# Kernel optimization log

Hardware: AMD Instinct MI355X
Metric: run time of the kernel (lower is better)

## Reference

```python
import jax, jax.numpy as jnp
import numpy as np

LN_EPS = 1e-5

def _layernorm(x, g, b):
    mu = jnp.mean(x, axis=-1, keepdims=True)
    var = jnp.var(x, axis=-1, keepdims=True)
    return (x - mu) * jax.lax.rsqrt(var + LN_EPS) * g + b

def setup_inputs() -> dict:
    key = jax.random.key(0)
    ks = jax.random.split(key, 12)
    B, E, R = 32, 64, 36
    Dt, Di, D = 768, 2048, 512
    s = 0.02
    return {
        "text_feats": jax.random.normal(ks[0], (B, E, Dt), jnp.float32),
        "image_feats": jax.random.normal(ks[1], (B, R, Di), jnp.float32),
        "W_text": jax.random.normal(ks[2], (Dt, D), jnp.float32) * s,
        "b_text": jnp.zeros((D,), jnp.float32),
        "g_text": jnp.ones((D,), jnp.float32),
        "beta_text": jnp.zeros((D,), jnp.float32),
        "W_img": jax.random.normal(ks[3], (Di, D), jnp.float32) * s,
        "b_img": jnp.zeros((D,), jnp.float32),
        "g_img": jnp.ones((D,), jnp.float32),
        "beta_img": jnp.zeros((D,), jnp.float32),
        "W1": jax.random.normal(ks[4], (2 * D, D), jnp.float32) * s,
        "b1": jnp.zeros((D,), jnp.float32),
        "W2": jax.random.normal(ks[5], (D, 1), jnp.float32) * s,
        "b2": jnp.zeros((1,), jnp.float32),
    }

def reference(text_feats, image_feats, W_text, b_text, g_text, beta_text,
              W_img, b_img, g_img, beta_img, W1, b1, W2, b2):
    B, E, _ = text_feats.shape
    R = image_feats.shape[1]
    D = W_text.shape[1]
    # projections: Linear -> ReLU -> LayerNorm
    text_aligned = _layernorm(jax.nn.relu(text_feats @ W_text + b_text), g_text, beta_text)   # [B,E,D]
    image_aligned = _layernorm(jax.nn.relu(image_feats @ W_img + b_img), g_img, beta_img)     # [B,R,D]
    # pairwise scorer: split W1 to avoid materializing the [B,E,R,2D] concat
    W1_t, W1_i = W1[:D], W1[D:]
    h_t = text_aligned @ W1_t                 # [B,E,D]
    h_i = image_aligned @ W1_i + b1           # [B,R,D]
    h = jax.nn.relu(h_t[:, :, None, :] + h_i[:, None, :, :])  # [B,E,R,D]
    scores_raw = jnp.squeeze(h @ W2, -1) + b2[0]               # [B,E,R]
    alignment_scores = jax.nn.sigmoid(scores_raw)
    # softmax over flattened (E*R) per batch
    w = jax.nn.softmax(alignment_scores.reshape(B, E * R), axis=1).reshape(B, E, R)
    # weighted sum over regions, mean over entities
    aggregated = jnp.einsum('ber,brd->bd', w, image_aligned) / E   # [B,D]
    return alignment_scores, aggregated
```

## Files before the change

kernel.cpp:

```cpp
#include <hip/hip_runtime.h>
#include <math.h>

#define LN_EPS 1e-5f

typedef __attribute__((ext_vector_type(8))) short bf16x8;
typedef __attribute__((ext_vector_type(4))) float f32x4;
typedef unsigned short ushort_t;
typedef unsigned int uint_t;

__device__ __forceinline__ ushort_t f2bf(float f) {
    uint_t u = __float_as_uint(f);
    u += 0x7FFF + ((u >> 16) & 1);
    return (ushort_t)(u >> 16);
}

__device__ __forceinline__ bf16x8 cvt8(float4 a, float4 b) {
    bf16x8 r;
    r[0] = (short)f2bf(a.x); r[1] = (short)f2bf(a.y);
    r[2] = (short)f2bf(a.z); r[3] = (short)f2bf(a.w);
    r[4] = (short)f2bf(b.x); r[5] = (short)f2bf(b.y);
    r[6] = (short)f2bf(b.z); r[7] = (short)f2bf(b.w);
    return r;
}

__global__ __launch_bounds__(256) void prep_kernel(
    const float* __restrict__ W_text, const float* __restrict__ W_img,
    const float* __restrict__ W1,
    ushort_t* __restrict__ Wt_t, ushort_t* __restrict__ Wi_t,
    ushort_t* __restrict__ W1t_t, ushort_t* __restrict__ W1i_t,
    float* __restrict__ stats)
{
    __shared__ float t[32][33];
    int local = blockIdx.x;
    if (local >= 1920) {
        for (int i = threadIdx.x; i < 6400; i += 256) stats[i] = 0.f;
        return;
    }
    const float* src; ushort_t* dst; int K;
    if      (local < 384)  { src = W_text;         dst = Wt_t;  K = 768;  }
    else if (local < 1408) { src = W_img;          dst = Wi_t;  K = 2048; local -= 384; }
    else if (local < 1664) { src = W1;             dst = W1t_t; K = 512;  local -= 1408; }
    else                   { src = W1 + 512 * 512; dst = W1i_t; K = 512;  local -= 1664; }
    const int ntk = K / 32;
    const int k0 = (local % ntk) * 32;
    const int n0 = (local / ntk) * 32;
    const int x = threadIdx.x % 32, y = threadIdx.x / 32;
    #pragma unroll
    for (int j = 0; j < 4; ++j)
        t[y + 8 * j][x] = src[(size_t)(k0 + y + 8 * j) * 512 + n0 + x];
    __syncthreads();
    #pragma unroll
    for (int j = 0; j < 4; ++j)
        dst[(size_t)(n0 + y + 8 * j) * K + k0 + x] = f2bf(t[x][y + 8 * j]);
}

__global__ __launch_bounds__(256) void proj_kernel(
    const float* __restrict__ A0, const ushort_t* __restrict__ B0,
    const float* __restrict__ bias0, float* __restrict__ C0, int K0,
    const float* __restrict__ A1, const ushort_t* __restrict__ B1,
    const float* __restrict__ bias1, float* __restrict__ C1, int K1,
    float* __restrict__ stats, int ysplit)
{
    __shared__ float red[4][64][64];

    const float* A; const ushort_t* Bt; const float* bias; float* C; int K, srow;
    int yy = blockIdx.y;
    if (yy < ysplit) { A = A0; Bt = B0; bias = bias0; C = C0; K = K0; srow = yy * 64; }
    else { A = A1; Bt = B1; bias = bias1; C = C1; K = K1; yy -= ysplit; srow = 2048 + yy * 64; }

    const int tid  = threadIdx.x;
    const int wave = tid >> 6;
    const int lane = tid & 63;
    const int q    = lane >> 4;
    const int mj   = lane & 15;
    const int brow = yy * 64;
    const int bcol = blockIdx.x * 64;

    const float*    Ab = A  + (size_t)(brow + mj) * K + q * 8;
    const ushort_t* Bb = Bt + (size_t)(bcol + mj) * K + q * 8;
    const int kw0    = wave * (K >> 2);
    const int ksteps = K >> 7;

    f32x4 acc[4][4] = {};

    #pragma unroll 2
    for (int s = 0; s < ksteps; ++s) {
        const int k = kw0 + s * 32;
        bf16x8 af[4], bf[4];
        #pragma unroll
        for (int i = 0; i < 4; ++i) {
            const float* pA = Ab + (size_t)i * 16 * K + k;
            float4 x0 = *(const float4*)pA;
            float4 x1 = *(const float4*)(pA + 4);
            af[i] = cvt8(x0, x1);
            bf[i] = *(const bf16x8*)(Bb + (size_t)i * 16 * K + k);
        }
        #pragma unroll
        for (int mi = 0; mi < 4; ++mi)
            #pragma unroll
            for (int ni = 0; ni < 4; ++ni)
                acc[mi][ni] = __builtin_amdgcn_mfma_f32_16x16x32_bf16(
                    af[mi], bf[ni], acc[mi][ni], 0, 0, 0);
    }

    #pragma unroll
    for (int mi = 0; mi < 4; ++mi)
        #pragma unroll
        for (int ni = 0; ni < 4; ++ni)
            #pragma unroll
            for (int r = 0; r < 4; ++r)
                red[wave][mi * 16 + q * 4 + r][ni * 16 + mj] = acc[mi][ni][r];
    __syncthreads();

    #pragma unroll
    for (int g = 0; g < 4; ++g) {
        const int idx = g * 1024 + tid * 4;
        const int row = idx >> 6, col = idx & 63;
        float4 v0 = *(float4*)&red[0][row][col];
        float4 v1 = *(float4*)&red[1][row][col];
        float4 v2 = *(float4*)&red[2][row][col];
        float4 v3 = *(float4*)&red[3][row][col];
        float4 bv = *(const float4*)&bias[bcol + col];
        float4 o;
        o.x = fmaxf((v0.x + v1.x) + (v2.x + v3.x) + bv.x, 0.f);
        o.y = fmaxf((v0.y + v1.y) + (v2.y + v3.y) + bv.y, 0.f);
        o.z = fmaxf((v0.z + v1.z) + (v2.z + v3.z) + bv.z, 0.f);
        o.w = fmaxf((v0.w + v1.w) + (v2.w + v3.w) + bv.w, 0.f);
        *(float4*)&C[(size_t)(brow + row) * 512 + bcol + col] = o;
        float s  = (o.x + o.y) + (o.z + o.w);
        float ss = (o.x * o.x + o.y * o.y) + (o.z * o.z + o.w * o.w);
        #pragma unroll
        for (int m = 1; m < 16; m <<= 1) {
            s  += __shfl_xor(s, m);
            ss += __shfl_xor(ss, m);
        }
        if ((tid & 15) == 0) {
            atomicAdd(&stats[(size_t)(srow + row) * 2], s);
            atomicAdd(&stats[(size_t)(srow + row) * 2 + 1], ss);
        }
    }
}

__global__ __launch_bounds__(256) void h_kernel(
    const float* __restrict__ A0, const ushort_t* __restrict__ B0,
    const float* __restrict__ bias0, float* __restrict__ C0,
    const float* __restrict__ g0, const float* __restrict__ be0, int soff0,
    const float* __restrict__ A1, const ushort_t* __restrict__ B1,
    const float* __restrict__ bias1, float* __restrict__ C1,
    const float* __restrict__ g1, const float* __restrict__ be1, int soff1,
    const float* __restrict__ stats, int ysplit)
{
    __shared__ float red[4][64][64];

    const float* A; const ushort_t* Bt; const float* bias; float* C;
    const float* g; const float* be; int soff;
    int yy = blockIdx.y;
    if (yy < ysplit) { A = A0; Bt = B0; bias = bias0; C = C0; g = g0; be = be0; soff = soff0; }
    else { A = A1; Bt = B1; bias = bias1; C = C1; g = g1; be = be1; soff = soff1; yy -= ysplit; }

    const int tid  = threadIdx.x;
    const int wave = tid >> 6;
    const int lane = tid & 63;
    const int q    = lane >> 4;
    const int mj   = lane & 15;
    const int brow = yy * 64;
    const int bcol = blockIdx.x * 64;

    float mu[4], rstd[4];
    #pragma unroll
    for (int i = 0; i < 4; ++i) {
        const int row = soff + brow + i * 16 + mj;
        float2 st = *(const float2*)&stats[(size_t)row * 2];
        float m   = st.x * (1.f / 512.f);
        float var = st.y * (1.f / 512.f) - m * m;
        mu[i] = m; rstd[i] = rsqrtf(var + LN_EPS);
    }

    const float*    Ab = A  + (size_t)(brow + mj) * 512 + q * 8;
    const ushort_t* Bb = Bt + (size_t)(bcol + mj) * 512 + q * 8;
    const int kw0 = wave * 128;

    f32x4 acc[4][4] = {};

    #pragma unroll 2
    for (int s = 0; s < 4; ++s) {
        const int k = kw0 + s * 32;
        float4 gv0 = *(const float4*)&g[k + q * 8];
        float4 gv1 = *(const float4*)&g[k + q * 8 + 4];
        float4 bv0 = *(const float4*)&be[k + q * 8];
        float4 bv1 = *(const float4*)&be[k + q * 8 + 4];
        bf16x8 af[4], bf[4];
        #pragma unroll
        for (int i = 0; i < 4; ++i) {
            const float* pA = Ab + (size_t)i * 16 * 512 + k;
            float4 x0 = *(const float4*)pA;
            float4 x1 = *(const float4*)(pA + 4);
            float4 t0, t1;
            t0.x = fmaf((x0.x - mu[i]) * rstd[i], gv0.x, bv0.x);
            t0.y = fmaf((x0.y - mu[i]) * rstd[i], gv0.y, bv0.y);
            t0.z = fmaf((x0.z - mu[i]) * rstd[i], gv0.z, bv0.z);
            t0.w = fmaf((x0.w - mu[i]) * rstd[i], gv0.w, bv0.w);
            t1.x = fmaf((x1.x - mu[i]) * rstd[i], gv1.x, bv1.x);
            t1.y = fmaf((x1.y - mu[i]) * rstd[i], gv1.y, bv1.y);
            t1.z = fmaf((x1.z - mu[i]) * rstd[i], gv1.z, bv1.z);
            t1.w = fmaf((x1.w - mu[i]) * rstd[i], gv1.w, bv1.w);
            af[i] = cvt8(t0, t1);
            bf[i] = *(const bf16x8*)(Bb + (size_t)i * 16 * 512 + k);
        }
        #pragma unroll
        for (int mi = 0; mi < 4; ++mi)
            #pragma unroll
            for (int ni = 0; ni < 4; ++ni)
                acc[mi][ni] = __builtin_amdgcn_mfma_f32_16x16x32_bf16(
                    af[mi], bf[ni], acc[mi][ni], 0, 0, 0);
    }

    #pragma unroll
    for (int mi = 0; mi < 4; ++mi)
        #pragma unroll
        for (int ni = 0; ni < 4; ++ni)
            #pragma unroll
            for (int r = 0; r < 4; ++r)
                red[wave][mi * 16 + q * 4 + r][ni * 16 + mj] = acc[mi][ni][r];
    __syncthreads();

    #pragma unroll
    for (int gq = 0; gq < 4; ++gq) {
        const int idx = gq * 1024 + tid * 4;
        const int row = idx >> 6, col = idx & 63;
        float4 v0 = *(float4*)&red[0][row][col];
        float4 v1 = *(float4*)&red[1][row][col];
        float4 v2 = *(float4*)&red[2][row][col];
        float4 v3 = *(float4*)&red[3][row][col];
        float4 o;
        o.x = (v0.x + v1.x) + (v2.x + v3.x);
        o.y = (v0.y + v1.y) + (v2.y + v3.y);
        o.z = (v0.z + v1.z) + (v2.z + v3.z);
        o.w = (v0.w + v1.w) + (v2.w + v3.w);
        if (bias) {
            float4 bv = *(const float4*)&bias[bcol + col];
            o.x += bv.x; o.y += bv.y; o.z += bv.z; o.w += bv.w;
        }
        *(float4*)&C[(size_t)(brow + row) * 512 + bcol + col] = o;
    }
}

__global__ __launch_bounds__(256) void scores_kernel(
    const float* __restrict__ ht, const float* __restrict__ hi,
    const float* __restrict__ W2, const float* __restrict__ b2,
    float* __restrict__ scores)
{
    const int blk  = blockIdx.x;
    const int b    = blk >> 4;
    const int e0   = (blk & 15) * 4;
    const int tid  = threadIdx.x;
    const int lane = tid & 63;
    const int wave = tid >> 6;

    float htv[4][8], w2v[8];
    #pragma unroll
    for (int e = 0; e < 4; ++e) {
        const float* htp = ht + (size_t)(b * 64 + e0 + e) * 512;
        #pragma unroll
        for (int j = 0; j < 8; ++j) htv[e][j] = htp[lane + 64 * j];
    }
    #pragma unroll
    for (int j = 0; j < 8; ++j) w2v[j] = W2[lane + 64 * j];
    const float bb = b2[0];
    const float* hib = hi + (size_t)b * 36 * 512;

    for (int r = wave; r < 36; r += 4) {
        const float* hir = hib + (size_t)r * 512;
        float hv[8];
        #pragma unroll
        for (int j = 0; j < 8; ++j) hv[j] = hir[lane + 64 * j];
        float a0 = 0.f, a1 = 0.f, a2 = 0.f, a3 = 0.f;
        #pragma unroll
        for (int j = 0; j < 8; ++j) {
            a0 = fmaf(fmaxf(htv[0][j] + hv[j], 0.f), w2v[j], a0);
            a1 = fmaf(fmaxf(htv[1][j] + hv[j], 0.f), w2v[j], a1);
            a2 = fmaf(fmaxf(htv[2][j] + hv[j], 0.f), w2v[j], a2);
            a3 = fmaf(fmaxf(htv[3][j] + hv[j], 0.f), w2v[j], a3);
        }
        #pragma unroll
        for (int off = 32; off; off >>= 1) {
            a0 += __shfl_down(a0, off);
            a1 += __shfl_down(a1, off);
            a2 += __shfl_down(a2, off);
            a3 += __shfl_down(a3, off);
        }
        if (lane == 0) {
            float* sp = scores + (size_t)(b * 64 + e0) * 36 + r;
            sp[0]      = 1.f / (1.f + expf(-(a0 + bb)));
            sp[36]     = 1.f / (1.f + expf(-(a1 + bb)));
            sp[72]     = 1.f / (1.f + expf(-(a2 + bb)));
            sp[108]    = 1.f / (1.f + expf(-(a3 + bb)));
        }
    }
}

__global__ __launch_bounds__(256) void agg_kernel(
    const float* __restrict__ scores, const float* __restrict__ ia_raw,
    const float* __restrict__ stats2,
    const float* __restrict__ g, const float* __restrict__ beta,
    float* __restrict__ outAgg)
{
    const int b   = blockIdx.x;
    const int tid = threadIdx.x;
    const float* sc = scores + (size_t)b * 2304;

    __shared__ float part[4][36];
    __shared__ float wsr[36];
    __shared__ float tmp[36];
    __shared__ float inv_s, c1_s;

    const int e4 = tid >> 6;
    const int r  = tid & 63;
    if (r < 36) {
        float p = 0.f;
        #pragma unroll
        for (int e = 0; e < 16; ++e) p += expf(sc[(e * 4 + e4) * 36 + r]);
        part[e4][r] = p;
    }
    __syncthreads();
    if (tid < 36) wsr[tid] = part[0][tid] + part[1][tid] + part[2][tid] + part[3][tid];
    __syncthreads();
    if (tid < 64) {
        float v = (tid < 36) ? wsr[tid] : 0.f;
        #pragma unroll
        for (int off = 32; off; off >>= 1) v += __shfl_down(v, off);
        if (tid == 0) inv_s = 1.f / (v * 64.f);
    }
    __syncthreads();
    if (tid < 36) {
        const int row = b * 36 + tid;
        float2 st = *(const float2*)&stats2[(size_t)row * 2];
        float m   = st.x * (1.f / 512.f);
        float var = st.y * (1.f / 512.f) - m * m;
        float rs  = rsqrtf(var + LN_EPS);
        float W   = wsr[tid] * inv_s;
        wsr[tid]  = W * rs;
        tmp[tid]  = W * rs * m;
    }
    __syncthreads();
    if (tid < 64) {
        float v = (tid < 36) ? tmp[tid] : 0.f;
        #pragma unroll
        for (int off = 32; off; off >>= 1) v += __shfl_down(v, off);
        if (tid == 0) c1_s = v;
    }
    __syncthreads();
    const float c1 = c1_s;

    const float* ib = ia_raw + (size_t)b * 36 * 512;
    for (int d = tid; d < 512; d += 256) {
        float acc = 0.f;
        #pragma unroll
        for (int rr = 0; rr < 36; ++rr)
            acc = fmaf(wsr[rr], ib[rr * 512 + d], acc);
        outAgg[(size_t)b * 512 + d] = g[d] * (acc - c1) + beta[d] * (1.f / 64.f);
    }
}

extern "C" void kernel_launch(void* const* d_in, const int* in_sizes, int n_in,
                              void* d_out, int out_size, void* d_ws, size_t ws_size,
                              hipStream_t stream)
{
    const float* text      = (const float*)d_in[0];
    const float* image     = (const float*)d_in[1];
    const float* W_text    = (const float*)d_in[2];
    const float* b_text    = (const float*)d_in[3];
    const float* g_text    = (const float*)d_in[4];
    const float* beta_text = (const float*)d_in[5];
    const float* W_img     = (const float*)d_in[6];
    const float* b_img     = (const float*)d_in[7];
    const float* g_img     = (const float*)d_in[8];
    const float* beta_img  = (const float*)d_in[9];
    const float* W1        = (const float*)d_in[10];
    const float* b1        = (const float*)d_in[11];
    const float* W2        = (const float*)d_in[12];
    const float* b2        = (const float*)d_in[13];

    float* out_scores = (float*)d_out;
    float* out_agg    = (float*)d_out + 73728;

    char* ws = (char*)d_ws;
    float*    ta    = (float*)(ws);
    float*    ia    = (float*)(ws + 4194304);
    float*    ht    = (float*)(ws + 6553600);
    float*    hi    = (float*)(ws + 10747904);
    ushort_t* Wt_t  = (ushort_t*)(ws + 13107200);
    ushort_t* Wi_t  = (ushort_t*)(ws + 13893632);
    ushort_t* W1t_t = (ushort_t*)(ws + 15990784);
    ushort_t* W1i_t = (ushort_t*)(ws + 16515072);
    float*    stats = (float*)(ws + 17039360);

    prep_kernel<<<1921, 256, 0, stream>>>(W_text, W_img, W1,
                                          Wt_t, Wi_t, W1t_t, W1i_t, stats);
    proj_kernel<<<dim3(8, 50), 256, 0, stream>>>(
        text, Wt_t, b_text, ta, 768,
        image, Wi_t, b_img, ia, 2048,
        stats, 32);
    h_kernel<<<dim3(8, 50), 256, 0, stream>>>(
        ta, W1t_t, nullptr, ht, g_text, beta_text, 0,
        ia, W1i_t, b1, hi, g_img, beta_img, 2048,
        stats, 32);
    scores_kernel<<<512, 256, 0, stream>>>(ht, hi, W2, b2, out_scores);
    agg_kernel<<<32, 256, 0, stream>>>(out_scores, ia, stats + 4096,
                                       g_img, beta_img, out_agg);
}
```

Baseline: 154.3 us.

## Fuse all stages into one cooperative persistent kernel with grid syncs

```diff
diff --git a/kernel.cpp b/kernel.cpp
--- a/kernel.cpp
+++ b/kernel.cpp
@@ -1,5 +1,8 @@
 #include <hip/hip_runtime.h>
+#include <hip/hip_cooperative_groups.h>
 #include <math.h>
+
+namespace cg = cooperative_groups;
 
 #define LN_EPS 1e-5f
 
@@ -23,342 +26,341 @@
     return r;
 }
 
-__global__ __launch_bounds__(256) void prep_kernel(
-    const float* __restrict__ W_text, const float* __restrict__ W_img,
-    const float* __restrict__ W1,
-    ushort_t* __restrict__ Wt_t, ushort_t* __restrict__ Wi_t,
-    ushort_t* __restrict__ W1t_t, ushort_t* __restrict__ W1i_t,
-    float* __restrict__ stats)
+__global__ void mega_kernel(
+    const float* __restrict__ text, const float* __restrict__ image,
+    const float* __restrict__ W_text, const float* __restrict__ b_text,
+    const float* __restrict__ g_text, const float* __restrict__ beta_text,
+    const float* __restrict__ W_img, const float* __restrict__ b_img,
+    const float* __restrict__ g_img, const float* __restrict__ beta_img,
+    const float* __restrict__ W1, const float* __restrict__ b1,
+    const float* __restrict__ W2, const float* __restrict__ b2,
+    float* __restrict__ out_scores, float* __restrict__ out_agg,
+    char* __restrict__ ws)
 {
-    __shared__ float t[32][33];
-    int local = blockIdx.x;
-    if (local >= 1920) {
-        for (int i = threadIdx.x; i < 6400; i += 256) stats[i] = 0.f;
-        return;
-    }
-    const float* src; ushort_t* dst; int K;
-    if      (local < 384)  { src = W_text;         dst = Wt_t;  K = 768;  }
-    else if (local < 1408) { src = W_img;          dst = Wi_t;  K = 2048; local -= 384; }
-    else if (local < 1664) { src = W1;             dst = W1t_t; K = 512;  local -= 1408; }
-    else                   { src = W1 + 512 * 512; dst = W1i_t; K = 512;  local -= 1664; }
-    const int ntk = K / 32;
-    const int k0 = (local % ntk) * 32;
-    const int n0 = (local / ntk) * 32;
-    const int x = threadIdx.x % 32, y = threadIdx.x / 32;
-    #pragma unroll
-    for (int j = 0; j < 4; ++j)
-        t[y + 8 * j][x] = src[(size_t)(k0 + y + 8 * j) * 512 + n0 + x];
-    __syncthreads();
-    #pragma unroll
-    for (int j = 0; j < 4; ++j)
-        dst[(size_t)(n0 + y + 8 * j) * K + k0 + x] = f2bf(t[x][y + 8 * j]);
-}
-
-__global__ __launch_bounds__(256) void proj_kernel(
-    const float* __restrict__ A0, const ushort_t* __restrict__ B0,
-    const float* __restrict__ bias0, float* __restrict__ C0, int K0,
-    const float* __restrict__ A1, const ushort_t* __restrict__ B1,
-    const float* __restrict__ bias1, float* __restrict__ C1, int K1,
-    float* __restrict__ stats, int ysplit)
-{
-    __shared__ float red[4][64][64];
-
-    const float* A; const ushort_t* Bt; const float* bias; float* C; int K, srow;
-    int yy = blockIdx.y;
-    if (yy < ysplit) { A = A0; Bt = B0; bias = bias0; C = C0; K = K0; srow = yy * 64; }
-    else { A = A1; Bt = B1; bias = bias1; C = C1; K = K1; yy -= ysplit; srow = 2048 + yy * 64; }
-
+    __shared__ __align__(16) float red[4][64][64];
+
+    ushort_t* text_bf  = (ushort_t*)(ws);
+    ushort_t* image_bf = (ushort_t*)(ws + 3145728);
+    float*    ta       = (float*)(ws + 7864320);
+    float*    ia       = (float*)(ws + 12058624);
+    float*    ht       = (float*)(ws + 14417920);
+    float*    hi       = (float*)(ws + 18612224);
+    ushort_t* Wt_t     = (ushort_t*)(ws + 20971520);
+    ushort_t* Wi_t     = (ushort_t*)(ws + 21757952);
+    ushort_t* W1t_t    = (ushort_t*)(ws + 23855104);
+    ushort_t* W1i_t    = (ushort_t*)(ws + 24379392);
+    float*    stats    = (float*)(ws + 24903680);
+
+    cg::grid_group gg = cg::this_grid();
     const int tid  = threadIdx.x;
     const int wave = tid >> 6;
     const int lane = tid & 63;
     const int q    = lane >> 4;
     const int mj   = lane & 15;
-    const int brow = yy * 64;
-    const int bcol = blockIdx.x * 64;
-
-    const float*    Ab = A  + (size_t)(brow + mj) * K + q * 8;
-    const ushort_t* Bb = Bt + (size_t)(bcol + mj) * K + q * 8;
-    const int kw0    = wave * (K >> 2);
-    const int ksteps = K >> 7;
-
-    f32x4 acc[4][4] = {};
-
-    #pragma unroll 2
-    for (int s = 0; s < ksteps; ++s) {
-        const int k = kw0 + s * 32;
-        bf16x8 af[4], bf[4];
+
+    for (int u = blockIdx.x; u < 5761; u += gridDim.x) {
+        if (u < 3840) {
+            const int i4 = u * 1024 + tid * 4;
+            const float* src; ushort_t* dst; int off;
+            if (i4 < 1572864) { src = text;  dst = text_bf;  off = i4; }
+            else              { src = image; dst = image_bf; off = i4 - 1572864; }
+            float4 v = *(const float4*)(src + off);
+            ushort4 o;
+            o.x = f2bf(v.x); o.y = f2bf(v.y); o.z = f2bf(v.z); o.w = f2bf(v.w);
+            *(ushort4*)(dst + off) = o;
+        } else if (u < 5760) {
+            float (*t33)[33] = (float(*)[33])&red[0][0][0];
+            int local = u - 3840;
+            const float* src; ushort_t* dst; int K;
+            if      (local < 384)  { src = W_text;         dst = Wt_t;  K = 768;  }
+            else if (local < 1408) { src = W_img;          dst = Wi_t;  K = 2048; local -= 384; }
+            else if (local < 1664) { src = W1;             dst = W1t_t; K = 512;  local -= 1408; }
+            else                   { src = W1 + 512 * 512; dst = W1i_t; K = 512;  local -= 1664; }
+            const int ntk = K / 32;
+            const int k0 = (local % ntk) * 32;
+            const int n0 = (local / ntk) * 32;
+            const int x = tid % 32, y = tid / 32;
+            __syncthreads();
+            #pragma unroll
+            for (int j = 0; j < 4; ++j)
+                t33[y + 8 * j][x] = src[(size_t)(k0 + y + 8 * j) * 512 + n0 + x];
+            __syncthreads();
+            #pragma unroll
+            for (int j = 0; j < 4; ++j)
+                dst[(size_t)(n0 + y + 8 * j) * K + k0 + x] = f2bf(t33[x][y + 8 * j]);
+        } else {
+            for (int i = tid; i < 6400; i += 256) stats[i] = 0.f;
+        }
+    }
+
+    gg.sync();
+    for (int u = blockIdx.x; u < 400; u += gridDim.x) {
+        const ushort_t* A; const ushort_t* Bt; const float* bias; float* C;
+        int K, srow, yy, xx;
+        if (u < 256) {
+            yy = u >> 3; xx = u & 7;
+            A = text_bf; Bt = Wt_t; bias = b_text; C = ta; K = 768; srow = yy * 64;
+        } else {
+            int v = u - 256; yy = v >> 3; xx = v & 7;
+            A = image_bf; Bt = Wi_t; bias = b_img; C = ia; K = 2048; srow = 2048 + yy * 64;
+        }
+        const int brow = yy * 64, bcol = xx * 64;
+        const ushort_t* Ab = A  + (size_t)(brow + mj) * K + q * 8;
+        const ushort_t* Bb = Bt + (size_t)(bcol + mj) * K + q * 8;
+        const int kw0 = wave * (K >> 2);
+        const int ksteps = K >> 7;
+
+        f32x4 acc[4][4] = {};
+        #pragma unroll 2
+        for (int s = 0; s < ksteps; ++s) {
+            const int k = kw0 + s * 32;
+            bf16x8 af[4], bfr[4];
+            #pragma unroll
+            for (int i = 0; i < 4; ++i) {
+                af[i]  = *(const bf16x8*)(Ab + (size_t)i * 16 * K + k);
+                bfr[i] = *(const bf16x8*)(Bb + (size_t)i * 16 * K + k);
+            }
+            #pragma unroll
+            for (int mi = 0; mi < 4; ++mi)
+                #pragma unroll
+                for (int ni = 0; ni < 4; ++ni)
+                    acc[mi][ni] = __builtin_amdgcn_mfma_f32_16x16x32_bf16(
+                        af[mi], bfr[ni], acc[mi][ni], 0, 0, 0);
+        }
+        #pragma unroll
+        for (int mi = 0; mi < 4; ++mi)
+            #pragma unroll
+            for (int ni = 0; ni < 4; ++ni)
+                #pragma unroll
+                for (int r = 0; r < 4; ++r)
+                    red[wave][mi * 16 + q * 4 + r][ni * 16 + mj] = acc[mi][ni][r];
+        __syncthreads();
+        #pragma unroll
+        for (int g4 = 0; g4 < 4; ++g4) {
+            const int idx = g4 * 1024 + tid * 4;
+            const int row = idx >> 6, col = idx & 63;
+            float4 v0 = *(float4*)&red[0][row][col];
+            float4 v1 = *(float4*)&red[1][row][col];
+            float4 v2 = *(float4*)&red[2][row][col];
+            float4 v3 = *(float4*)&red[3][row][col];
+            float4 bv = *(const float4*)&bias[bcol + col];
+            float4 o;
+            o.x = fmaxf((v0.x + v1.x) + (v2.x + v3.x) + bv.x, 0.f);
+            o.y = fmaxf((v0.y + v1.y) + (v2.y + v3.y) + bv.y, 0.f);
+            o.z = fmaxf((v0.z + v1.z) + (v2.z + v3.z) + bv.z, 0.f);
+            o.w = fmaxf((v0.w + v1.w) + (v2.w + v3.w) + bv.w, 0.f);
+            *(float4*)&C[(size_t)(brow + row) * 512 + bcol + col] = o;
+            float s  = (o.x + o.y) + (o.z + o.w);
+            float ss = (o.x * o.x + o.y * o.y) + (o.z * o.z + o.w * o.w);
+            #pragma unroll
+            for (int m = 1; m < 16; m <<= 1) {
+                s  += __shfl_xor(s, m);
+                ss += __shfl_xor(ss, m);
+            }
+            if ((tid & 15) == 0) {
+                atomicAdd(&stats[(size_t)(srow + row) * 2], s);
+                atomicAdd(&stats[(size_t)(srow + row) * 2 + 1], ss);
+            }
+        }
+        __syncthreads();
+    }
+
+    gg.sync();
+    for (int u = blockIdx.x; u < 400; u += gridDim.x) {
+        const float* A; const ushort_t* Bt; const float* bias; float* C;
+        const float* g; const float* be; int soff, yy, xx;
+        if (u < 256) {
+            yy = u >> 3; xx = u & 7;
+            A = ta; Bt = W1t_t; bias = nullptr; C = ht;
+            g = g_text; be = beta_text; soff = 0;
+        } else {
+            int v = u - 256; yy = v >> 3; xx = v & 7;
+            A = ia; Bt = W1i_t; bias = b1; C = hi;
+            g = g_img; be = beta_img; soff = 2048;
+        }
+        const int brow = yy * 64, bcol = xx * 64;
+
+        float mu[4], rstd[4];
         #pragma unroll
         for (int i = 0; i < 4; ++i) {
-            const float* pA = Ab + (size_t)i * 16 * K + k;
-            float4 x0 = *(const float4*)pA;
-            float4 x1 = *(const float4*)(pA + 4);
-            af[i] = cvt8(x0, x1);
-            bf[i] = *(const bf16x8*)(Bb + (size_t)i * 16 * K + k);
+            const int row = soff + brow + i * 16 + mj;
+            float2 st = *(const float2*)&stats[(size_t)row * 2];
+            float m   = st.x * (1.f / 512.f);
+            float var = st.y * (1.f / 512.f) - m * m;
+            mu[i] = m; rstd[i] = rsqrtf(var + LN_EPS);
+        }
+
+        const float*    Ab = A  + (size_t)(brow + mj) * 512 + q * 8;
+        const ushort_t* Bb = Bt + (size_t)(bcol + mj) * 512 + q * 8;
+        const int kw0 = wave * 128;
+
+        f32x4 acc[4][4] = {};
+        #pragma unroll 2
+        for (int s = 0; s < 4; ++s) {
+            const int k = kw0 + s * 32;
+            float4 gv0 = *(const float4*)&g[k + q * 8];
+            float4 gv1 = *(const float4*)&g[k + q * 8 + 4];
+            float4 bv0 = *(const float4*)&be[k + q * 8];
+            float4 bv1 = *(const float4*)&be[k + q * 8 + 4];
+            bf16x8 af[4], bfr[4];
+            #pragma unroll
+            for (int i = 0; i < 4; ++i) {
+                const float* pA = Ab + (size_t)i * 16 * 512 + k;
+                float4 x0 = *(const float4*)pA;
+                float4 x1 = *(const float4*)(pA + 4);
+                float4 t0, t1;
+                t0.x = fmaf((x0.x - mu[i]) * rstd[i], gv0.x, bv0.x);
+                t0.y = fmaf((x0.y - mu[i]) * rstd[i], gv0.y, bv0.y);
+                t0.z = fmaf((x0.z - mu[i]) * rstd[i], gv0.z, bv0.z);
+                t0.w = fmaf((x0.w - mu[i]) * rstd[i], gv0.w, bv0.w);
+                t1.x = fmaf((x1.x - mu[i]) * rstd[i], gv1.x, bv1.x);
+                t1.y = fmaf((x1.y - mu[i]) * rstd[i], gv1.y, bv1.y);
+                t1.z = fmaf((x1.z - mu[i]) * rstd[i], gv1.z, bv1.z);
+                t1.w = fmaf((x1.w - mu[i]) * rstd[i], gv1.w, bv1.w);
+                af[i]  = cvt8(t0, t1);
+                bfr[i] = *(const bf16x8*)(Bb + (size_t)i * 16 * 512 + k);
+            }
+            #pragma unroll
+            for (int mi = 0; mi < 4; ++mi)
+                #pragma unroll
+                for (int ni = 0; ni < 4; ++ni)
+                    acc[mi][ni] = __builtin_amdgcn_mfma_f32_16x16x32_bf16(
+                        af[mi], bfr[ni], acc[mi][ni], 0, 0, 0);
         }
         #pragma unroll
         for (int mi = 0; mi < 4; ++mi)
             #pragma unroll
             for (int ni = 0; ni < 4; ++ni)
-                acc[mi][ni] = __builtin_amdgcn_mfma_f32_16x16x32_bf16(
-                    af[mi], bf[ni], acc[mi][ni], 0, 0, 0);
-    }
-
-    #pragma unroll
-    for (int mi = 0; mi < 4; ++mi)
-        #pragma unroll
-        for (int ni = 0; ni < 4; ++ni)
-            #pragma unroll
-            for (int r = 0; r < 4; ++r)
-                red[wave][mi * 16 + q * 4 + r][ni * 16 + mj] = acc[mi][ni][r];
-    __syncthreads();
-
-    #pragma unroll
-    for (int g = 0; g < 4; ++g) {
-        const int idx = g * 1024 + tid * 4;
-        const int row = idx >> 6, col = idx & 63;
-        float4 v0 = *(float4*)&red[0][row][col];
-        float4 v1 = *(float4*)&red[1][row][col];
-        float4 v2 = *(float4*)&red[2][row][col];
-        float4 v3 = *(float4*)&red[3][row][col];
-        float4 bv = *(const float4*)&bias[bcol + col];
-        float4 o;
-        o.x = fmaxf((v0.x + v1.x) + (v2.x + v3.x) + bv.x, 0.f);
-        o.y = fmaxf((v0.y + v1.y) + (v2.y + v3.y) + bv.y, 0.f);
-        o.z = fmaxf((v0.z + v1.z) + (v2.z + v3.z) + bv.z, 0.f);
-        o.w = fmaxf((v0.w + v1.w) + (v2.w + v3.w) + bv.w, 0.f);
-        *(float4*)&C[(size_t)(brow + row) * 512 + bcol + col] = o;
-        float s  = (o.x + o.y) + (o.z + o.w);
-        float ss = (o.x * o.x + o.y * o.y) + (o.z * o.z + o.w * o.w);
-        #pragma unroll
-        for (int m = 1; m < 16; m <<= 1) {
-            s  += __shfl_xor(s, m);
-            ss += __shfl_xor(ss, m);
-        }
-        if ((tid & 15) == 0) {
-            atomicAdd(&stats[(size_t)(srow + row) * 2], s);
-            atomicAdd(&stats[(size_t)(srow + row) * 2 + 1], ss);
-        }
-    }
-}
-
-__global__ __launch_bounds__(256) void h_kernel(
-    const float* __restrict__ A0, const ushort_t* __restrict__ B0,
-    const float* __restrict__ bias0, float* __restrict__ C0,
-    const float* __restrict__ g0, const float* __restrict__ be0, int soff0,
-    const float* __restrict__ A1, const ushort_t* __restrict__ B1,
-    const float* __restrict__ bias1, float* __restrict__ C1,
-    const float* __restrict__ g1, const float* __restrict__ be1, int soff1,
-    const float* __restrict__ stats, int ysplit)
-{
-    __shared__ float red[4][64][64];
-
-    const float* A; const ushort_t* Bt; const float* bias; float* C;
-    const float* g; const float* be; int soff;
-    int yy = blockIdx.y;
-    if (yy < ysplit) { A = A0; Bt = B0; bias = bias0; C = C0; g = g0; be = be0; soff = soff0; }
-    else { A = A1; Bt = B1; bias = bias1; C = C1; g = g1; be = be1; soff = soff1; yy -= ysplit; }
-
-    const int tid  = threadIdx.x;
-    const int wave = tid >> 6;
-    const int lane = tid & 63;
-    const int q    = lane >> 4;
-    const int mj   = lane & 15;
-    const int brow = yy * 64;
-    const int bcol = blockIdx.x * 64;
-
-    float mu[4], rstd[4];
-    #pragma unroll
-    for (int i = 0; i < 4; ++i) {
-        const int row = soff + brow + i * 16 + mj;
-        float2 st = *(const float2*)&stats[(size_t)row * 2];
-        float m   = st.x * (1.f / 512.f);
-        float var = st.y * (1.f / 512.f) - m * m;
-        mu[i] = m; rstd[i] = rsqrtf(var + LN_EPS);
-    }
-
-    const float*    Ab = A  + (size_t)(brow + mj) * 512 + q * 8;
-    const ushort_t* Bb = Bt + (size_t)(bcol + mj) * 512 + q * 8;
-    const int kw0 = wave * 128;
-
-    f32x4 acc[4][4] = {};
-
-    #pragma unroll 2
-    for (int s = 0; s < 4; ++s) {
-        const int k = kw0 + s * 32;
-        float4 gv0 = *(const float4*)&g[k + q * 8];
-        float4 gv1 = *(const float4*)&g[k + q * 8 + 4];
-        float4 bv0 = *(const float4*)&be[k + q * 8];
-        float4 bv1 = *(const float4*)&be[k + q * 8 + 4];
-        bf16x8 af[4], bf[4];
-        #pragma unroll
-        for (int i = 0; i < 4; ++i) {
-            const float* pA = Ab + (size_t)i * 16 * 512 + k;
-            float4 x0 = *(const float4*)pA;
-            float4 x1 = *(const float4*)(pA + 4);
-            float4 t0, t1;
-            t0.x = fmaf((x0.x - mu[i]) * rstd[i], gv0.x, bv0.x);
-            t0.y = fmaf((x0.y - mu[i]) * rstd[i], gv0.y, bv0.y);
-            t0.z = fmaf((x0.z - mu[i]) * rstd[i], gv0.z, bv0.z);
-            t0.w = fmaf((x0.w - mu[i]) * rstd[i], gv0.w, bv0.w);
-            t1.x = fmaf((x1.x - mu[i]) * rstd[i], gv1.x, bv1.x);
-            t1.y = fmaf((x1.y - mu[i]) * rstd[i], gv1.y, bv1.y);
-            t1.z = fmaf((x1.z - mu[i]) * rstd[i], gv1.z, bv1.z);
-            t1.w = fmaf((x1.w - mu[i]) * rstd[i], gv1.w, bv1.w);
-            af[i] = cvt8(t0, t1);
-            bf[i] = *(const bf16x8*)(Bb + (size_t)i * 16 * 512 + k);
-        }
-        #pragma unroll
-        for (int mi = 0; mi < 4; ++mi)
-            #pragma unroll
-            for (int ni = 0; ni < 4; ++ni)
-                acc[mi][ni] = __builtin_amdgcn_mfma_f32_16x16x32_bf16(
-                    af[mi], bf[ni], acc[mi][ni], 0, 0, 0);
-    }
-
-    #pragma unroll
-    for (int mi = 0; mi < 4; ++mi)
-        #pragma unroll
-        for (int ni = 0; ni < 4; ++ni)
-            #pragma unroll
-            for (int r = 0; r < 4; ++r)
-                red[wave][mi * 16 + q * 4 + r][ni * 16 + mj] = acc[mi][ni][r];
-    __syncthreads();
-
-    #pragma unroll
-    for (int gq = 0; gq < 4; ++gq) {
-        const int idx = gq * 1024 + tid * 4;
-        const int row = idx >> 6, col = idx & 63;
-        float4 v0 = *(float4*)&red[0][row][col];
-        float4 v1 = *(float4*)&red[1][row][col];
-        float4 v2 = *(float4*)&red[2][row][col];
-        float4 v3 = *(float4*)&red[3][row][col];
-        float4 o;
-        o.x = (v0.x + v1.x) + (v2.x + v3.x);
-        o.y = (v0.y + v1.y) + (v2.y + v3.y);
-        o.z = (v0.z + v1.z) + (v2.z + v3.z);
-        o.w = (v0.w + v1.w) + (v2.w + v3.w);
-        if (bias) {
-            float4 bv = *(const float4*)&bias[bcol + col];
-            o.x += bv.x; o.y += bv.y; o.z += bv.z; o.w += bv.w;
-        }
-        *(float4*)&C[(size_t)(brow + row) * 512 + bcol + col] = o;
-    }
-}
-
-__global__ __launch_bounds__(256) void scores_kernel(
-    const float* __restrict__ ht, const float* __restrict__ hi,
-    const float* __restrict__ W2, const float* __restrict__ b2,
-    float* __restrict__ scores)
-{
-    const int blk  = blockIdx.x;
-    const int b    = blk >> 4;
-    const int e0   = (blk & 15) * 4;
-    const int tid  = threadIdx.x;
-    const int lane = tid & 63;
-    const int wave = tid >> 6;
-
-    float htv[4][8], w2v[8];
-    #pragma unroll
-    for (int e = 0; e < 4; ++e) {
-        const float* htp = ht + (size_t)(b * 64 + e0 + e) * 512;
-        #pragma unroll
-        for (int j = 0; j < 8; ++j) htv[e][j] = htp[lane + 64 * j];
-    }
-    #pragma unroll
-    for (int j = 0; j < 8; ++j) w2v[j] = W2[lane + 64 * j];
-    const float bb = b2[0];
-    const float* hib = hi + (size_t)b * 36 * 512;
-
-    for (int r = wave; r < 36; r += 4) {
-        const float* hir = hib + (size_t)r * 512;
-        float hv[8];
-        #pragma unroll
-        for (int j = 0; j < 8; ++j) hv[j] = hir[lane + 64 * j];
-        float a0 = 0.f, a1 = 0.f, a2 = 0.f, a3 = 0.f;
-        #pragma unroll
-        for (int j = 0; j < 8; ++j) {
-            a0 = fmaf(fmaxf(htv[0][j] + hv[j], 0.f), w2v[j], a0);
-            a1 = fmaf(fmaxf(htv[1][j] + hv[j], 0.f), w2v[j], a1);
-            a2 = fmaf(fmaxf(htv[2][j] + hv[j], 0.f), w2v[j], a2);
-            a3 = fmaf(fmaxf(htv[3][j] + hv[j], 0.f), w2v[j], a3);
-        }
-        #pragma unroll
-        for (int off = 32; off; off >>= 1) {
-            a0 += __shfl_down(a0, off);
-            a1 += __shfl_down(a1, off);
-            a2 += __shfl_down(a2, off);
-            a3 += __shfl_down(a3, off);
-        }
-        if (lane == 0) {
-            float* sp = scores + (size_t)(b * 64 + e0) * 36 + r;
-            sp[0]      = 1.f / (1.f + expf(-(a0 + bb)));
-            sp[36]     = 1.f / (1.f + expf(-(a1 + bb)));
-            sp[72]     = 1.f / (1.f + expf(-(a2 + bb)));
-            sp[108]    = 1.f / (1.f + expf(-(a3 + bb)));
-        }
-    }
-}
-
-__global__ __launch_bounds__(256) void agg_kernel(
-    const float* __restrict__ scores, const float* __restrict__ ia_raw,
-    const float* __restrict__ stats2,
-    const float* __restrict__ g, const float* __restrict__ beta,
-    float* __restrict__ outAgg)
-{
-    const int b   = blockIdx.x;
-    const int tid = threadIdx.x;
-    const float* sc = scores + (size_t)b * 2304;
-
-    __shared__ float part[4][36];
-    __shared__ float wsr[36];
-    __shared__ float tmp[36];
-    __shared__ float inv_s, c1_s;
-
-    const int e4 = tid >> 6;
-    const int r  = tid & 63;
-    if (r < 36) {
-        float p = 0.f;
-        #pragma unroll
-        for (int e = 0; e < 16; ++e) p += expf(sc[(e * 4 + e4) * 36 + r]);
-        part[e4][r] = p;
-    }
-    __syncthreads();
-    if (tid < 36) wsr[tid] = part[0][tid] + part[1][tid] + part[2][tid] + part[3][tid];
-    __syncthreads();
-    if (tid < 64) {
-        float v = (tid < 36) ? wsr[tid] : 0.f;
-        #pragma unroll
-        for (int off = 32; off; off >>= 1) v += __shfl_down(v, off);
-        if (tid == 0) inv_s = 1.f / (v * 64.f);
-    }
-    __syncthreads();
-    if (tid < 36) {
-        const int row = b * 36 + tid;
-        float2 st = *(const float2*)&stats2[(size_t)row * 2];
-        float m   = st.x * (1.f / 512.f);
-        float var = st.y * (1.f / 512.f) - m * m;
-        float rs  = rsqrtf(var + LN_EPS);
-        float W   = wsr[tid] * inv_s;
-        wsr[tid]  = W * rs;
-        tmp[tid]  = W * rs * m;
-    }
-    __syncthreads();
-    if (tid < 64) {
-        float v = (tid < 36) ? tmp[tid] : 0.f;
-        #pragma unroll
-        for (int off = 32; off; off >>= 1) v += __shfl_down(v, off);
-        if (tid == 0) c1_s = v;
-    }
-    __syncthreads();
-    const float c1 = c1_s;
-
-    const float* ib = ia_raw + (size_t)b * 36 * 512;
-    for (int d = tid; d < 512; d += 256) {
-        float acc = 0.f;
-        #pragma unroll
-        for (int rr = 0; rr < 36; ++rr)
-            acc = fmaf(wsr[rr], ib[rr * 512 + d], acc);
-        outAgg[(size_t)b * 512 + d] = g[d] * (acc - c1) + beta[d] * (1.f / 64.f);
+                #pragma unroll
+                for (int r = 0; r < 4; ++r)
+                    red[wave][mi * 16 + q * 4 + r][ni * 16 + mj] = acc[mi][ni][r];
+        __syncthreads();
+        #pragma unroll
+        for (int g4 = 0; g4 < 4; ++g4) {
+            const int idx = g4 * 1024 + tid * 4;
+            const int row = idx >> 6, col = idx & 63;
+            float4 v0 = *(float4*)&red[0][row][col];
+            float4 v1 = *(float4*)&red[1][row][col];
+            float4 v2 = *(float4*)&red[2][row][col];
+            float4 v3 = *(float4*)&red[3][row][col];
+            float4 o;
+            o.x = (v0.x + v1.x) + (v2.x + v3.x);
+            o.y = (v0.y + v1.y) + (v2.y + v3.y);
+            o.z = (v0.z + v1.z) + (v2.z + v3.z);
+            o.w = (v0.w + v1.w) + (v2.w + v3.w);
+            if (bias) {
+                float4 bv = *(const float4*)&bias[bcol + col];
+                o.x += bv.x; o.y += bv.y; o.z += bv.z; o.w += bv.w;
+            }
+            *(float4*)&C[(size_t)(brow + row) * 512 + bcol + col] = o;
+        }
+        __syncthreads();
+    }
+
+    gg.sync();
+    for (int u = blockIdx.x; u < 512; u += gridDim.x) {
+        const int b  = u >> 4;
+        const int e0 = (u & 15) * 4;
+        float htv[4][8], w2v[8];
+        #pragma unroll
+        for (int e = 0; e < 4; ++e) {
+            const float* htp = ht + (size_t)(b * 64 + e0 + e) * 512;
+            #pragma unroll
+            for (int j = 0; j < 8; ++j) htv[e][j] = htp[lane + 64 * j];
+        }
+        #pragma unroll
+        for (int j = 0; j < 8; ++j) w2v[j] = W2[lane + 64 * j];
+        const float bb = b2[0];
+        const float* hib = hi + (size_t)b * 36 * 512;
+
+        for (int r = wave; r < 36; r += 4) {
+            const float* hir = hib + (size_t)r * 512;
+            float hv[8];
+            #pragma unroll
+            for (int j = 0; j < 8; ++j) hv[j] = hir[lane + 64 * j];
+            float a0 = 0.f, a1 = 0.f, a2 = 0.f, a3 = 0.f;
+            #pragma unroll
+            for (int j = 0; j < 8; ++j) {
+                a0 = fmaf(fmaxf(htv[0][j] + hv[j], 0.f), w2v[j], a0);
+                a1 = fmaf(fmaxf(htv[1][j] + hv[j], 0.f), w2v[j], a1);
+                a2 = fmaf(fmaxf(htv[2][j] + hv[j], 0.f), w2v[j], a2);
+                a3 = fmaf(fmaxf(htv[3][j] + hv[j], 0.f), w2v[j], a3);
+            }
+            #pragma unroll
+            for (int off = 32; off; off >>= 1) {
+                a0 += __shfl_down(a0, off);
+                a1 += __shfl_down(a1, off);
+                a2 += __shfl_down(a2, off);
+                a3 += __shfl_down(a3, off);
+            }
+            if (lane == 0) {
+                float* sp = out_scores + (size_t)(b * 64 + e0) * 36 + r;
+                sp[0]   = 1.f / (1.f + expf(-(a0 + bb)));
+                sp[36]  = 1.f / (1.f + expf(-(a1 + bb)));
+                sp[72]  = 1.f / (1.f + expf(-(a2 + bb)));
+                sp[108] = 1.f / (1.f + expf(-(a3 + bb)));
+            }
+        }
+    }
+
+    gg.sync();
+    for (int u = blockIdx.x; u < 256; u += gridDim.x) {
+        const int b  = u >> 3;
+        const int d0 = (u & 7) * 64;
+        const float* sc = out_scores + (size_t)b * 2304;
+        float (*part)[36] = (float(*)[36])&red[0][0][0];
+        float* wsr = &red[1][0][0];
+        float* tmp = &red[2][0][0];
+        float* msc = &red[3][0][0];
+
+        const int e4 = tid >> 6;
+        const int r  = tid & 63;
+        __syncthreads();
+        if (r < 36) {
+            float p = 0.f;
+            #pragma unroll
+            for (int e = 0; e < 16; ++e) p += expf(sc[(e * 4 + e4) * 36 + r]);
+            part[e4][r] = p;
+        }
+        __syncthreads();
+        if (tid < 36) wsr[tid] = part[0][tid] + part[1][tid] + part[2][tid] + part[3][tid];
+        __syncthreads();
+        if (tid < 64) {
+            float v = (tid < 36) ? wsr[tid] : 0.f;
+            #pragma unroll
+            for (int off = 32; off; off >>= 1) v += __shfl_down(v, off);
+            if (tid == 0) msc[0] = 1.f / (v * 64.f);
+        }
+        __syncthreads();
+        if (tid < 36) {
+            const int row = b * 36 + tid;
+            float2 st = *(const float2*)&stats[(size_t)(2048 + row) * 2];
+            float m   = st.x * (1.f / 512.f);
+            float var = st.y * (1.f / 512.f) - m * m;
+            float rs  = rsqrtf(var + LN_EPS);
+            float W   = wsr[tid] * msc[0];
+            wsr[tid]  = W * rs;
+            tmp[tid]  = W * rs * m;
+        }
+        __syncthreads();
+        if (tid < 64) {
+            float v = (tid < 36) ? tmp[tid] : 0.f;
+            #pragma unroll
+            for (int off = 32; off; off >>= 1) v += __shfl_down(v, off);
+            if (tid == 0) msc[1] = v;
+        }
+        __syncthreads();
+        if (tid < 64) {
+            const int d = d0 + tid;
+            const float c1 = msc[1];
+            const float* ib = ia + (size_t)b * 36 * 512;
+            float acc = 0.f;
+            #pragma unroll
+            for (int rr = 0; rr < 36; ++rr)
+                acc = fmaf(wsr[rr], ib[rr * 512 + d], acc);
+            out_agg[(size_t)b * 512 + d] = g_img[d] * (acc - c1) + beta_img[d] * (1.f / 64.f);
+        }
+        __syncthreads();
     }
 }
 
@@ -383,29 +385,24 @@
 
     float* out_scores = (float*)d_out;
     float* out_agg    = (float*)d_out + 73728;
-
-    char* ws = (char*)d_ws;
-    float*    ta    = (float*)(ws);
-    float*    ia    = (float*)(ws + 4194304);
-    float*    ht    = (float*)(ws + 6553600);
-    float*    hi    = (float*)(ws + 10747904);
-    ushort_t* Wt_t  = (ushort_t*)(ws + 13107200);
-    ushort_t* Wi_t  = (ushort_t*)(ws + 13893632);
-    ushort_t* W1t_t = (ushort_t*)(ws + 15990784);
-    ushort_t* W1i_t = (ushort_t*)(ws + 16515072);
-    float*    stats = (float*)(ws + 17039360);
-
-    prep_kernel<<<1921, 256, 0, stream>>>(W_text, W_img, W1,
-                                          Wt_t, Wi_t, W1t_t, W1i_t, stats);
-    proj_kernel<<<dim3(8, 50), 256, 0, stream>>>(
-        text, Wt_t, b_text, ta, 768,
-        image, Wi_t, b_img, ia, 2048,
-        stats, 32);
-    h_kernel<<<dim3(8, 50), 256, 0, stream>>>(
-        ta, W1t_t, nullptr, ht, g_text, beta_text, 0,
-        ia, W1i_t, b1, hi, g_img, beta_img, 2048,
-        stats, 32);
-    scores_kernel<<<512, 256, 0, stream>>>(ht, hi, W2, b2, out_scores);
-    agg_kernel<<<32, 256, 0, stream>>>(out_scores, ia, stats + 4096,
-                                       g_img, beta_img, out_agg);
+    char*  wsc        = (char*)d_ws;
+
+    int maxPerCU = 0;
+    hipError_t err = hipOccupancyMaxActiveBlocksPerMultiprocessor(
+        &maxPerCU, mega_kernel, 256, 0);
+    int nblk = 512;
+    if (err == hipSuccess && maxPerCU > 0) {
+        int cap = maxPerCU * 256;
+        if (cap < nblk) nblk = cap;
+    }
+
+    void* args[17] = {
+        (void*)&text, (void*)&image,
+        (void*)&W_text, (void*)&b_text, (void*)&g_text, (void*)&beta_text,
+        (void*)&W_img, (void*)&b_img, (void*)&g_img, (void*)&beta_img,
+        (void*)&W1, (void*)&b1, (void*)&W2, (void*)&b2,
+        (void*)&out_scores, (void*)&out_agg, (void*)&wsc
+    };
+    hipLaunchCooperativeKernel((void*)mega_kernel, dim3(nblk), dim3(256),
+                               args, 0, stream);
 }
```

Result: slower. 437.0 us (+183.3%).
